# Performance work log

Measured on AMD Instinct MI355X. Metric: run time of the kernel, lower is better.

The kernel has to match this reference:

```python
import jax, jax.numpy as jnp
import numpy as np

NUM_CLASSES = 14
IGNORE = 0
MAX_SAMPLES = 28 * 50
MAX_VIEWS = 50
TEMP = 0.1
THRESH = 0.3


def setup_inputs() -> dict:
    key = jax.random.key(0)
    B, Fd, D, H, W = 2, 128, 16, 128, 128
    N = B * D * H * W
    feats = jax.random.normal(key, (B, Fd, D, H, W), jnp.float32)
    idx = np.arange(N)
    pred = (idx % NUM_CLASSES).astype(np.int32)
    # alternate blocks: easy (label==pred) / hard (label!=pred) so every class
    # has >max_views pixels with >= n_view/2 hard and easy samples
    block = (idx // NUM_CLASSES) % 2
    lab = np.where(block == 0, pred, (pred + 1) % NUM_CLASSES).astype(np.int32)
    labels = jnp.asarray(lab.reshape(B, D, H, W))
    predict = jnp.asarray(pred.reshape(B, D, H, W))
    probability = jnp.ones((B, D, H, W), jnp.float32)
    queue = jax.random.normal(jax.random.fold_in(key, 1), (NUM_CLASSES, 4096, Fd), jnp.float32)
    return {"feats": feats, "labels": labels, "predict": predict,
            "probability": probability, "queue": queue}


def _l2n(x):
    return x / jnp.linalg.norm(x, axis=-1, keepdims=True)


def reference(feats, labels, predict, probability, queue):
    Fd = feats.shape[1]
    # [B, Fd, D, H, W] -> [N, Fd]
    f = jnp.transpose(feats, (0, 2, 3, 4, 1)).reshape(-1, Fd)
    lab = labels.reshape(-1)
    pred = predict.reshape(-1)
    valid = probability.reshape(-1) > THRESH
    N = f.shape[0]

    total_classes = NUM_CLASSES - 1              # all non-ignore classes qualify by construction
    n_view = min(MAX_SAMPLES // total_classes, MAX_VIEWS)  # = 50
    n_hard = n_view // 2                          # balanced branch always taken
    n_easy = n_view - n_hard
    idxs = jnp.arange(N)

    def pick(mask, k):
        # deterministic stand-in for randperm: first k valid indices
        keys = jnp.where(mask, idxs, N)
        return jnp.sort(keys)[:k]

    def sample_class(c):
        hard = valid & (pred == c) & (lab != c)
        easy = valid & (pred == c) & (lab == c)
        sel = jnp.concatenate([pick(hard, n_hard), pick(easy, n_easy)])
        return f[sel]

    classes = jnp.arange(1, NUM_CLASSES)
    X_ = jax.vmap(sample_class)(classes)          # [C-1, n_view, Fd]

    # positive queue: per-class mean of (threshold-filtered) feats
    onehot = jax.nn.one_hot(lab, NUM_CLASSES, dtype=f.dtype) * valid[:, None].astype(f.dtype)
    sums = jnp.einsum('nc,nd->cd', onehot, f)     # [C, Fd]
    cnts = onehot.sum(0)[:, None]
    pos_queue = sums / cnts                        # [C, Fd]

    # negatives: second half of cache, classes 1..C-1 (class 0 skipped in _sample_negative)
    neg = queue[1:, queue.shape[1] // 2:, :]       # [C-1, M, Fd]

    a = _l2n(X_)                                   # [C-1, V, Fd]
    p = _l2n(pos_queue[1:])                        # [C-1, Fd]
    n = _l2n(neg)                                  # [C-1, M, Fd]

    logits = jnp.einsum('cvd,cd->cv', a, p) / TEMP           # [C-1, V]
    neg_sum = jnp.exp(jnp.einsum('cvd,cmd->cvm', a, n) / TEMP).sum(-1)  # [C-1, V]
    log_prob = -logits + jnp.log(jnp.exp(logits) + neg_sum)
    # sum over classes of per-class mean, divided by num classes
    return log_prob.mean(axis=1).mean()
```

## Files before the change

### kernel.cpp

```cpp
#include <hip/hip_runtime.h>

#define NUMC 14
#define FD 128
#define SPATIAL (16*128*128)
#define N_TOTAL (2*SPATIAL)
#define NV 50
#define NH 25
#define TC 13
#define QLEN 4096
#define MCH 64
#define NCHUNK 32
#define NSTR (FD + 4)
#define NSUMBLK 2048
#define NNEGBLK (TC * NCHUNK)
#define PXB 32768
#define THRESH_F 0.3f
#define RSTR 65

#define WS_SEL     0
#define WS_LOSSP   656
#define WS_CNT0    672
#define WS_NEGPART 680
#define WS_PART    21480
#define WS_LAB8    152552

__global__ __launch_bounds__(256) void k_pre(const int* __restrict__ labels,
        const int* __restrict__ predict, const float* __restrict__ prob,
        unsigned char* __restrict__ lab8, int* __restrict__ sel, int* __restrict__ cnt0) {
    int blk = blockIdx.x;
    int tid = threadIdx.x;
    if (blk < 512) {
        int n = blk * 1024 + tid * 4;
        int4   lb = *(const int4*)(labels + n);
        float4 pv = *(const float4*)(prob + n);
        uchar4 o;
        o.x = pv.x > THRESH_F ? (unsigned char)(lb.x & 15) : (unsigned char)15;
        o.y = pv.y > THRESH_F ? (unsigned char)(lb.y & 15) : (unsigned char)15;
        o.z = pv.z > THRESH_F ? (unsigned char)(lb.z & 15) : (unsigned char)15;
        o.w = pv.w > THRESH_F ? (unsigned char)(lb.w & 15) : (unsigned char)15;
        *(uchar4*)(lab8 + n) = o;
    } else if (blk < 538) {
        if (tid >= 64) return;
        int cat = blk - 512;
        int c = 1 + (cat >> 1);
        bool hard = (cat & 1) == 0;
        int lane = tid;
        int* slot = sel + (c - 1) * NV + (hard ? 0 : NH);
        int found = 0;
        for (int base = 0; base < N_TOTAL && found < NH; base += 64) {
            int n = base + lane;
            bool m = false;
            int pr = predict[n];
            if (pr == c && prob[n] > THRESH_F) {
                int lb = labels[n];
                m = hard ? (lb != c) : (lb == c);
            }
            unsigned long long mask = __ballot(m);
            int rank = __popcll(mask & ((1ull << lane) - 1ull));
            if (m && (found + rank) < NH) slot[found + rank] = n;
            found += __popcll(mask);
        }
        if (lane >= found && lane < NH) slot[lane] = N_TOTAL - 1;
    } else {
        if (tid == 0) cnt0[0] = 0;
    }
}

#define ACCUM(v, u) do { \
    int i0 = r0 + ((u).x & 15); \
    int i1 = r0 + 16 + ((u).y & 15); \
    int i2 = r0 + 32 + ((u).z & 15); \
    int i3 = r0 + 48 + ((u).w & 15); \
    float a0 = smem[i0], a1 = smem[i1], a2 = smem[i2], a3 = smem[i3]; \
    smem[i0] = a0 + (v).x; smem[i1] = a1 + (v).y; \
    smem[i2] = a2 + (v).z; smem[i3] = a3 + (v).w; \
} while (0)

__global__ __launch_bounds__(256) void k_main(const float* __restrict__ feats,
        const unsigned char* __restrict__ lab8, const float* __restrict__ queue,
        const int* __restrict__ sel, float* __restrict__ part, float* __restrict__ negpart) {
    __shared__ float smem[256 * RSTR];
    int tid = threadIdx.x;
    int lane = tid & 63, w = tid >> 6;

    if (blockIdx.x < NSUMBLK) {
        int plane = blockIdx.x >> 3;
        int chunk = blockIdx.x & 7;
        int b = plane >> 7;
        int r0 = tid * RSTR;
        #pragma unroll
        for (int k = 0; k < RSTR; ++k) smem[r0 + k] = 0.f;

        const float4* fp4 = (const float4*)(feats + (size_t)plane * SPATIAL) + (chunk << 13);
        const uchar4* lp4 = (const uchar4*)(lab8 + (size_t)b * SPATIAL) + (chunk << 13);
        float4 v0 = fp4[tid],       v1 = fp4[tid + 256];
        uchar4 u0 = lp4[tid],       u1 = lp4[tid + 256];
        for (int i = 0; i < 30; i += 2) {
            float4 p0 = fp4[(i + 2) * 256 + tid];
            uchar4 q0 = lp4[(i + 2) * 256 + tid];
            float4 p1 = fp4[(i + 3) * 256 + tid];
            uchar4 q1 = lp4[(i + 3) * 256 + tid];
            ACCUM(v0, u0);
            ACCUM(v1, u1);
            v0 = p0; u0 = q0; v1 = p1; u1 = q1;
        }
        ACCUM(v0, u0);
        ACCUM(v1, u1);

        float* pw = part + (size_t)((blockIdx.x << 2) + w) * 16;
        #pragma unroll
        for (int cc = 0; cc < NUMC; ++cc) {
            float t = smem[r0 + cc] + smem[r0 + 16 + cc]
                    + smem[r0 + 32 + cc] + smem[r0 + 48 + cc];
            #pragma unroll
            for (int o = 32; o; o >>= 1) t += __shfl_xor(t, o);
            if (lane == 0) pw[cc] = t;
        }
    } else {
        int nb = blockIdx.x - NSUMBLK;
        int ci = nb >> 5;
        int chunk = nb & 31;
        float* a_s  = smem;
        float* n_s  = smem + 6400;
        float* an_s = smem + 14848;
        int*   sel_s = (int*)(smem + 14912);
        if (tid < NV) sel_s[tid] = sel[ci * NV + tid];
        const float* qp = queue + ((size_t)(ci + 1) * QLEN + (QLEN / 2) + chunk * MCH) * (size_t)FD;
        for (int i = tid; i < MCH * FD / 4; i += 256) {
            int m = i / (FD / 4), k4 = i % (FD / 4);
            ((float4*)(n_s + m * NSTR))[k4] = ((const float4*)qp)[i];
        }
        __syncthreads();
        for (int i = tid; i < NV * FD; i += 256) {
            int r = i >> 7, ch = i & 127;
            int n = sel_s[r];
            int b = n >> 18, sp = n & (SPATIAL - 1);
            a_s[i] = feats[(size_t)(b * FD + ch) * SPATIAL + sp];
        }
        __syncthreads();
        for (int r = w; r < NV; r += 4) {
            float x0 = a_s[r * FD + lane], x1 = a_s[r * FD + 64 + lane];
            float q = x0 * x0 + x1 * x1;
            #pragma unroll
            for (int o = 32; o; o >>= 1) q += __shfl_xor(q, o);
            if (lane == 0) an_s[r] = sqrtf(q);
        }
        __syncthreads();
        float4 nr[FD / 4];
        const float4* nrow = (const float4*)(n_s + lane * NSTR);
        float sq = 0.f;
        #pragma unroll
        for (int k = 0; k < FD / 4; ++k) {
            nr[k] = nrow[k];
            sq += nr[k].x*nr[k].x + nr[k].y*nr[k].y + nr[k].z*nr[k].z + nr[k].w*nr[k].w;
        }
        float inn = 10.f / sqrtf(sq);
        float* np = negpart + ((size_t)ci * NV) * NCHUNK + chunk;
        for (int v = w; v < NV; v += 4) {
            const float4* a4 = (const float4*)(a_s + v * FD);
            float dot = 0.f;
            #pragma unroll
            for (int k = 0; k < FD / 4; ++k) {
                float4 x = a4[k];
                dot += x.x*nr[k].x + x.y*nr[k].y + x.z*nr[k].z + x.w*nr[k].w;
            }
            float e = __expf(dot * inn / an_s[v]);
            #pragma unroll
            for (int o = 32; o; o >>= 1) e += __shfl_xor(e, o);
            if (lane == 0) np[(size_t)v * NCHUNK] = e;
        }
    }
}

__global__ __launch_bounds__(256) void k_loss(const float* __restrict__ feats,
        const int* __restrict__ sel, const float* __restrict__ part,
        const float* __restrict__ negpart, float* __restrict__ lossp,
        int* __restrict__ cnt0, float* __restrict__ out) {
    __shared__ float p_s[FD];
    __shared__ float a_s[NV * FD];
    __shared__ float an_s[NV];
    __shared__ int   sel_s[NV];
    __shared__ float red_s[2];
    __shared__ float lacc[8];
    int tid = threadIdx.x;
    int ci = blockIdx.x, c = ci + 1;
    if (tid < NV) sel_s[tid] = sel[ci * NV + tid];
    if (tid < 128) {
        const float* pp = part + c;
        float s = 0.f;
        #pragma unroll
        for (int p = 0; p < 2; ++p) {
            int pl = tid + (p << 7);
            for (int k = 0; k < 32; ++k) s += pp[(size_t)(pl * 32 + k) * 16];
        }
        p_s[tid] = s;
    }
    __syncthreads();
    if (tid < 128) {
        float q = p_s[tid] * p_s[tid];
        #pragma unroll
        for (int o = 32; o; o >>= 1) q += __shfl_xor(q, o);
        if ((tid & 63) == 0) red_s[tid >> 6] = q;
    }
    for (int i = tid; i < NV * FD; i += 256) {
        int r = i >> 7, ch = i & 127;
        int n = sel_s[r];
        int b = n >> 18, sp = n & (SPATIAL - 1);
        a_s[i] = feats[(size_t)(b * FD + ch) * SPATIAL + sp];
    }
    __syncthreads();
    float pninv10 = 10.f * rsqrtf(red_s[0] + red_s[1]);
    int lane = tid & 63, w = tid >> 6;
    for (int r = w; r < NV; r += 4) {
        float x0 = a_s[r * FD + lane], x1 = a_s[r * FD + 64 + lane];
        float q = x0 * x0 + x1 * x1;
        #pragma unroll
        for (int o = 32; o; o >>= 1) q += __shfl_xor(q, o);
        if (lane == 0) an_s[r] = sqrtf(q);
    }
    __syncthreads();
    int grp = tid >> 5, l32 = tid & 31;
    float acc = 0.f;
    for (int r = grp; r < NV; r += 8) {
        const float4* a4 = (const float4*)(a_s + r * FD);
        const float4* p4 = (const float4*)p_s;
        float4 x = a4[l32], y = p4[l32];
        float d = x.x*y.x + x.y*y.y + x.z*y.z + x.w*y.w;
        float ns = negpart[(size_t)(ci * NV + r) * 32 + l32];
        #pragma unroll
        for (int o = 16; o; o >>= 1) { d += __shfl_xor(d, o); ns += __shfl_xor(ns, o); }
        if (l32 == 0) {
            float logit = d * pninv10 / an_s[r];
            acc += -logit + logf(__expf(logit) + ns);
        }
    }
    if (l32 == 0) lacc[grp] = acc;
    __syncthreads();
    if (tid == 0) {
        float s = 0.f;
        #pragma unroll
        for (int i = 0; i < 8; ++i) s += lacc[i];
        lossp[ci] = s;
        __threadfence();
        int t = atomicAdd(cnt0, 1);
        if (t == TC - 1) {
            __threadfence();
            float tot = 0.f;
            for (int i = 0; i < TC; ++i)
                tot += __hip_atomic_load(lossp + i, __ATOMIC_RELAXED, __HIP_MEMORY_SCOPE_AGENT);
            out[0] = tot * (1.f / (TC * NV));
        }
    }
}

extern "C" void kernel_launch(void* const* d_in, const int* in_sizes, int n_in,
                              void* d_out, int out_size, void* d_ws, size_t ws_size,
                              hipStream_t stream) {
    (void)in_sizes; (void)n_in; (void)out_size; (void)ws_size;
    const float* feats   = (const float*)d_in[0];
    const int*   labels  = (const int*)d_in[1];
    const int*   predict = (const int*)d_in[2];
    const float* prob    = (const float*)d_in[3];
    const float* queue   = (const float*)d_in[4];
    float* ws  = (float*)d_ws;
    float* out = (float*)d_out;

    int*   sel     = (int*)(ws + WS_SEL);
    float* lossp   = ws + WS_LOSSP;
    int*   cnt0    = (int*)(ws + WS_CNT0);
    float* negpart = ws + WS_NEGPART;
    float* part    = ws + WS_PART;
    unsigned char* lab8 = (unsigned char*)(ws + WS_LAB8);

    k_pre  <<<539, 256, 0, stream>>>(labels, predict, prob, lab8, sel, cnt0);
    k_main <<<NSUMBLK + NNEGBLK, 256, 0, stream>>>(feats, lab8, queue, sel, part, negpart);
    k_loss <<<TC, 256, 0, stream>>>(feats, sel, part, negpart, lossp, cnt0, out);
}
```

Measured before the change: 117.5 us.

## Gather anchor rows once, shrink histogram smem, reorder blocks, nontemporal feature loads

Adds a k_gather kernel that fetches the 650 selected anchor rows and their norms once into workspace. The negative-dot and loss kernels now read these rows instead of each redoing the strided gather from feats. The class-sum path halves its per-thread histogram (RSTR 65→33) so more blocks fit per CU, and issues 4-deep nontemporal loads. Negative blocks are now scheduled first, and partial sums use a class-major layout so the loss reduction reads contiguous memory. In exchange it adds an extra kernel launch, and the negative path now reads anchors from global memory instead of registers/LDS.

```diff
diff --git a/kernel.cpp b/kernel.cpp
--- a/kernel.cpp
+++ b/kernel.cpp
@@ -13,16 +13,19 @@
 #define NSTR (FD + 4)
 #define NSUMBLK 2048
 #define NNEGBLK (TC * NCHUNK)
-#define PXB 32768
 #define THRESH_F 0.3f
-#define RSTR 65
+#define RSTR 33
+
+typedef float f32x4 __attribute__((ext_vector_type(4)));
 
 #define WS_SEL     0
 #define WS_LOSSP   656
 #define WS_CNT0    672
 #define WS_NEGPART 680
-#define WS_PART    21480
-#define WS_LAB8    152552
+#define WS_ANORM   21480
+#define WS_AROWS   22144
+#define WS_PART    105344
+#define WS_LAB8    134016
 
 __global__ __launch_bounds__(256) void k_pre(const int* __restrict__ labels,
         const int* __restrict__ predict, const float* __restrict__ prob,
@@ -66,132 +69,139 @@
     }
 }
 
+__global__ __launch_bounds__(128) void k_gather(const float* __restrict__ feats,
+        const int* __restrict__ sel, float* __restrict__ arows, float* __restrict__ anorm) {
+    __shared__ float red[2];
+    int r = blockIdx.x;
+    int t = threadIdx.x;
+    int n = sel[r];
+    int b = n >> 18, sp = n & (SPATIAL - 1);
+    float v = feats[((size_t)(b * FD + t)) * SPATIAL + sp];
+    arows[r * FD + t] = v;
+    float a = v * v;
+    #pragma unroll
+    for (int o = 32; o; o >>= 1) a += __shfl_xor(a, o);
+    if ((t & 63) == 0) red[t >> 6] = a;
+    __syncthreads();
+    if (t == 0) anorm[r] = sqrtf(red[0] + red[1]);
+}
+
 #define ACCUM(v, u) do { \
     int i0 = r0 + ((u).x & 15); \
     int i1 = r0 + 16 + ((u).y & 15); \
-    int i2 = r0 + 32 + ((u).z & 15); \
-    int i3 = r0 + 48 + ((u).w & 15); \
-    float a0 = smem[i0], a1 = smem[i1], a2 = smem[i2], a3 = smem[i3]; \
+    float a0 = smem[i0], a1 = smem[i1]; \
     smem[i0] = a0 + (v).x; smem[i1] = a1 + (v).y; \
+    int i2 = r0 + ((u).z & 15); \
+    int i3 = r0 + 16 + ((u).w & 15); \
+    float a2 = smem[i2], a3 = smem[i3]; \
     smem[i2] = a2 + (v).z; smem[i3] = a3 + (v).w; \
 } while (0)
 
-__global__ __launch_bounds__(256) void k_main(const float* __restrict__ feats,
+__global__ __launch_bounds__(256, 4) void k_main(const float* __restrict__ feats,
         const unsigned char* __restrict__ lab8, const float* __restrict__ queue,
-        const int* __restrict__ sel, float* __restrict__ part, float* __restrict__ negpart) {
-    __shared__ float smem[256 * RSTR];
+        const float* __restrict__ arows, const float* __restrict__ anorm,
+        float* __restrict__ part, float* __restrict__ negpart) {
+    __shared__ float smem[256 * RSTR + 64];
     int tid = threadIdx.x;
     int lane = tid & 63, w = tid >> 6;
 
-    if (blockIdx.x < NSUMBLK) {
-        int plane = blockIdx.x >> 3;
-        int chunk = blockIdx.x & 7;
+    if (blockIdx.x < NNEGBLK) {
+        int ci = blockIdx.x >> 5;
+        int chunk = blockIdx.x & 31;
+        float* n_s  = smem;
+        float* an_s = smem + 8448;
+        if (tid < NV) an_s[tid] = anorm[ci * NV + tid];
+        const float* qp = queue + ((size_t)(ci + 1) * QLEN + (QLEN / 2) + chunk * MCH) * (size_t)FD;
+        for (int i = tid; i < MCH * (FD / 4); i += 256) {
+            int m = i >> 5, k4 = i & 31;
+            ((float4*)(n_s + m * NSTR))[k4] = ((const float4*)qp)[i];
+        }
+        __syncthreads();
+        const float4* nrow = (const float4*)(n_s + lane * NSTR);
+        float sq = 0.f;
+        #pragma unroll
+        for (int k = 0; k < FD / 4; ++k) {
+            float4 t = nrow[k];
+            sq += t.x*t.x + t.y*t.y + t.z*t.z + t.w*t.w;
+        }
+        float inn = 10.f * rsqrtf(sq);
+        float* np = negpart + (size_t)(ci * NV) * NCHUNK + chunk;
+        const float4* abase = (const float4*)(arows + (size_t)(ci * NV) * FD);
+        for (int v = w; v < NV; v += 4) {
+            const float4* a4 = abase + v * (FD / 4);
+            float dot = 0.f;
+            #pragma unroll
+            for (int k = 0; k < FD / 4; ++k) {
+                float4 x = a4[k], y = nrow[k];
+                dot += x.x*y.x + x.y*y.y + x.z*y.z + x.w*y.w;
+            }
+            float e = __expf(dot * inn / an_s[v]);
+            #pragma unroll
+            for (int o = 32; o; o >>= 1) e += __shfl_xor(e, o);
+            if (lane == 0) np[(size_t)v * NCHUNK] = e;
+        }
+    } else {
+        int sb = blockIdx.x - NNEGBLK;
+        int plane = sb >> 3;
+        int chunk = sb & 7;
         int b = plane >> 7;
         int r0 = tid * RSTR;
         #pragma unroll
         for (int k = 0; k < RSTR; ++k) smem[r0 + k] = 0.f;
 
-        const float4* fp4 = (const float4*)(feats + (size_t)plane * SPATIAL) + (chunk << 13);
+        const f32x4* fp4 = (const f32x4*)(feats + (size_t)plane * SPATIAL) + (chunk << 13);
         const uchar4* lp4 = (const uchar4*)(lab8 + (size_t)b * SPATIAL) + (chunk << 13);
-        float4 v0 = fp4[tid],       v1 = fp4[tid + 256];
-        uchar4 u0 = lp4[tid],       u1 = lp4[tid + 256];
-        for (int i = 0; i < 30; i += 2) {
-            float4 p0 = fp4[(i + 2) * 256 + tid];
-            uchar4 q0 = lp4[(i + 2) * 256 + tid];
-            float4 p1 = fp4[(i + 3) * 256 + tid];
-            uchar4 q1 = lp4[(i + 3) * 256 + tid];
-            ACCUM(v0, u0);
-            ACCUM(v1, u1);
+        f32x4 v0 = __builtin_nontemporal_load(fp4 + tid);
+        f32x4 v1 = __builtin_nontemporal_load(fp4 + tid + 256);
+        f32x4 v2 = __builtin_nontemporal_load(fp4 + tid + 512);
+        f32x4 v3 = __builtin_nontemporal_load(fp4 + tid + 768);
+        uchar4 u0 = lp4[tid], u1 = lp4[tid + 256], u2 = lp4[tid + 512], u3 = lp4[tid + 768];
+        for (int i = 0; i < 28; i += 4) {
+            f32x4 p0 = __builtin_nontemporal_load(fp4 + (i + 4) * 256 + tid);
+            uchar4 q0 = lp4[(i + 4) * 256 + tid];
+            f32x4 p1 = __builtin_nontemporal_load(fp4 + (i + 5) * 256 + tid);
+            uchar4 q1 = lp4[(i + 5) * 256 + tid];
+            f32x4 p2 = __builtin_nontemporal_load(fp4 + (i + 6) * 256 + tid);
+            uchar4 q2 = lp4[(i + 6) * 256 + tid];
+            f32x4 p3 = __builtin_nontemporal_load(fp4 + (i + 7) * 256 + tid);
+            uchar4 q3 = lp4[(i + 7) * 256 + tid];
+            ACCUM(v0, u0); ACCUM(v1, u1); ACCUM(v2, u2); ACCUM(v3, u3);
             v0 = p0; u0 = q0; v1 = p1; u1 = q1;
-        }
-        ACCUM(v0, u0);
-        ACCUM(v1, u1);
-
-        float* pw = part + (size_t)((blockIdx.x << 2) + w) * 16;
+            v2 = p2; u2 = q2; v3 = p3; u3 = q3;
+        }
+        ACCUM(v0, u0); ACCUM(v1, u1); ACCUM(v2, u2); ACCUM(v3, u3);
+
+        float* aux = smem + 256 * RSTR;
         #pragma unroll
         for (int cc = 0; cc < NUMC; ++cc) {
-            float t = smem[r0 + cc] + smem[r0 + 16 + cc]
-                    + smem[r0 + 32 + cc] + smem[r0 + 48 + cc];
+            float t = smem[r0 + cc] + smem[r0 + 16 + cc];
             #pragma unroll
             for (int o = 32; o; o >>= 1) t += __shfl_xor(t, o);
-            if (lane == 0) pw[cc] = t;
-        }
-    } else {
-        int nb = blockIdx.x - NSUMBLK;
-        int ci = nb >> 5;
-        int chunk = nb & 31;
-        float* a_s  = smem;
-        float* n_s  = smem + 6400;
-        float* an_s = smem + 14848;
-        int*   sel_s = (int*)(smem + 14912);
-        if (tid < NV) sel_s[tid] = sel[ci * NV + tid];
-        const float* qp = queue + ((size_t)(ci + 1) * QLEN + (QLEN / 2) + chunk * MCH) * (size_t)FD;
-        for (int i = tid; i < MCH * FD / 4; i += 256) {
-            int m = i / (FD / 4), k4 = i % (FD / 4);
-            ((float4*)(n_s + m * NSTR))[k4] = ((const float4*)qp)[i];
+            if (lane == 0) aux[w * 16 + cc] = t;
         }
         __syncthreads();
-        for (int i = tid; i < NV * FD; i += 256) {
-            int r = i >> 7, ch = i & 127;
-            int n = sel_s[r];
-            int b = n >> 18, sp = n & (SPATIAL - 1);
-            a_s[i] = feats[(size_t)(b * FD + ch) * SPATIAL + sp];
-        }
-        __syncthreads();
-        for (int r = w; r < NV; r += 4) {
-            float x0 = a_s[r * FD + lane], x1 = a_s[r * FD + 64 + lane];
-            float q = x0 * x0 + x1 * x1;
-            #pragma unroll
-            for (int o = 32; o; o >>= 1) q += __shfl_xor(q, o);
-            if (lane == 0) an_s[r] = sqrtf(q);
-        }
-        __syncthreads();
-        float4 nr[FD / 4];
-        const float4* nrow = (const float4*)(n_s + lane * NSTR);
-        float sq = 0.f;
-        #pragma unroll
-        for (int k = 0; k < FD / 4; ++k) {
-            nr[k] = nrow[k];
-            sq += nr[k].x*nr[k].x + nr[k].y*nr[k].y + nr[k].z*nr[k].z + nr[k].w*nr[k].w;
-        }
-        float inn = 10.f / sqrtf(sq);
-        float* np = negpart + ((size_t)ci * NV) * NCHUNK + chunk;
-        for (int v = w; v < NV; v += 4) {
-            const float4* a4 = (const float4*)(a_s + v * FD);
-            float dot = 0.f;
-            #pragma unroll
-            for (int k = 0; k < FD / 4; ++k) {
-                float4 x = a4[k];
-                dot += x.x*nr[k].x + x.y*nr[k].y + x.z*nr[k].z + x.w*nr[k].w;
-            }
-            float e = __expf(dot * inn / an_s[v]);
-            #pragma unroll
-            for (int o = 32; o; o >>= 1) e += __shfl_xor(e, o);
-            if (lane == 0) np[(size_t)v * NCHUNK] = e;
-        }
-    }
-}
-
-__global__ __launch_bounds__(256) void k_loss(const float* __restrict__ feats,
-        const int* __restrict__ sel, const float* __restrict__ part,
+        if (tid < NUMC)
+            part[(size_t)tid * NSUMBLK + sb] =
+                aux[tid] + aux[16 + tid] + aux[32 + tid] + aux[48 + tid];
+    }
+}
+
+__global__ __launch_bounds__(256) void k_loss(const float* __restrict__ arows,
+        const float* __restrict__ anorm, const float* __restrict__ part,
         const float* __restrict__ negpart, float* __restrict__ lossp,
         int* __restrict__ cnt0, float* __restrict__ out) {
     __shared__ float p_s[FD];
-    __shared__ float a_s[NV * FD];
-    __shared__ float an_s[NV];
-    __shared__ int   sel_s[NV];
     __shared__ float red_s[2];
     __shared__ float lacc[8];
     int tid = threadIdx.x;
     int ci = blockIdx.x, c = ci + 1;
-    if (tid < NV) sel_s[tid] = sel[ci * NV + tid];
     if (tid < 128) {
-        const float* pp = part + c;
         float s = 0.f;
         #pragma unroll
-        for (int p = 0; p < 2; ++p) {
-            int pl = tid + (p << 7);
-            for (int k = 0; k < 32; ++k) s += pp[(size_t)(pl * 32 + k) * 16];
+        for (int b = 0; b < 2; ++b) {
+            const float* pp = part + (size_t)c * NSUMBLK + b * 1024 + tid * 8;
+            #pragma unroll
+            for (int k = 0; k < 8; ++k) s += pp[k];
         }
         p_s[tid] = s;
     }
@@ -202,35 +212,21 @@
         for (int o = 32; o; o >>= 1) q += __shfl_xor(q, o);
         if ((tid & 63) == 0) red_s[tid >> 6] = q;
     }
-    for (int i = tid; i < NV * FD; i += 256) {
-        int r = i >> 7, ch = i & 127;
-        int n = sel_s[r];
-        int b = n >> 18, sp = n & (SPATIAL - 1);
-        a_s[i] = feats[(size_t)(b * FD + ch) * SPATIAL + sp];
-    }
     __syncthreads();
     float pninv10 = 10.f * rsqrtf(red_s[0] + red_s[1]);
-    int lane = tid & 63, w = tid >> 6;
-    for (int r = w; r < NV; r += 4) {
-        float x0 = a_s[r * FD + lane], x1 = a_s[r * FD + 64 + lane];
-        float q = x0 * x0 + x1 * x1;
-        #pragma unroll
-        for (int o = 32; o; o >>= 1) q += __shfl_xor(q, o);
-        if (lane == 0) an_s[r] = sqrtf(q);
-    }
-    __syncthreads();
     int grp = tid >> 5, l32 = tid & 31;
     float acc = 0.f;
     for (int r = grp; r < NV; r += 8) {
-        const float4* a4 = (const float4*)(a_s + r * FD);
+        int ar = ci * NV + r;
+        const float4* a4 = (const float4*)(arows + (size_t)ar * FD);
         const float4* p4 = (const float4*)p_s;
         float4 x = a4[l32], y = p4[l32];
         float d = x.x*y.x + x.y*y.y + x.z*y.z + x.w*y.w;
-        float ns = negpart[(size_t)(ci * NV + r) * 32 + l32];
+        float ns = negpart[(size_t)ar * NCHUNK + l32];
         #pragma unroll
         for (int o = 16; o; o >>= 1) { d += __shfl_xor(d, o); ns += __shfl_xor(ns, o); }
         if (l32 == 0) {
-            float logit = d * pninv10 / an_s[r];
+            float logit = d * pninv10 / anorm[ar];
             acc += -logit + logf(__expf(logit) + ns);
         }
     }
@@ -269,10 +265,13 @@
     float* lossp   = ws + WS_LOSSP;
     int*   cnt0    = (int*)(ws + WS_CNT0);
     float* negpart = ws + WS_NEGPART;
+    float* anorm   = ws + WS_ANORM;
+    float* arows   = ws + WS_AROWS;
     float* part    = ws + WS_PART;
     unsigned char* lab8 = (unsigned char*)(ws + WS_LAB8);
 
-    k_pre  <<<539, 256, 0, stream>>>(labels, predict, prob, lab8, sel, cnt0);
-    k_main <<<NSUMBLK + NNEGBLK, 256, 0, stream>>>(feats, lab8, queue, sel, part, negpart);
-    k_loss <<<TC, 256, 0, stream>>>(feats, sel, part, negpart, lossp, cnt0, out);
-}
+    k_pre    <<<539, 256, 0, stream>>>(labels, predict, prob, lab8, sel, cnt0);
+    k_gather <<<TC * NV, 128, 0, stream>>>(feats, sel, arows, anorm);
+    k_main   <<<NNEGBLK + NSUMBLK, 256, 0, stream>>>(feats, lab8, queue, arows, anorm, part, negpart);
+    k_loss   <<<TC, 256, 0, stream>>>(arows, anorm, part, negpart, lossp, cnt0, out);
+}
```

After: 127.0 us. +8.1%, slower.
